# Kernel tuning notes

Hardware: AMD Instinct MI355X
Metric: run time of the kernel (lower is better)

The kernel has to match this reference:

```python
import jax, jax.numpy as jnp
import numpy as np

WH, WW = 8, 8          # window height/width
N = WH * WW            # tokens per window = 64
DIM = 256              # channels
H = 8                  # heads
HD = DIM // H          # head dim = 32
NW = 1024              # number of windows per image (256/8)^2
B_ = 4096              # num_windows * batch (batch=4)
EPS = 1e-12            # F.normalize eps


def _rel_pos_index():
    # (2,Wh,Ww) coords -> pairwise relative index into bias table, shape (N, N)
    coords = np.stack(np.meshgrid(np.arange(WH), np.arange(WW), indexing='ij'))
    flat = coords.reshape(2, -1)                      # (2, N)
    rel = flat[:, :, None] - flat[:, None, :]         # (2, N, N)
    rel = rel.transpose(1, 2, 0).astype(np.int64)     # (N, N, 2)
    rel[..., 0] += WH - 1
    rel[..., 1] += WW - 1
    rel[..., 0] *= 2 * WW - 1
    return jnp.asarray(rel.sum(-1))                   # (N, N)

_RPI = _rel_pos_index()


def setup_inputs() -> dict:
    key = jax.random.key(0)
    ks = jax.random.split(key, 12)
    x = jax.random.normal(ks[0], (B_, N, DIM), dtype=jnp.float32)
    c = jax.random.normal(ks[1], (B_, N, DIM), dtype=jnp.float32)
    # 0 / -100 additive shifted-window mask, shape (nW, N, N)
    mask = jnp.where(jax.random.uniform(ks[2], (NW, N, N)) < 0.15, -100.0, 0.0).astype(jnp.float32)
    q_w = jax.random.normal(ks[3], (DIM, DIM), dtype=jnp.float32) * 0.02
    q_b = jnp.zeros((DIM,), jnp.float32)
    kv_w = jax.random.normal(ks[4], (2 * DIM, DIM), dtype=jnp.float32) * 0.02
    kv_b = jnp.zeros((2 * DIM,), jnp.float32)
    logit_scale = jnp.log(10.0) * jnp.ones((H, 1, 1), jnp.float32)
    rpb_table = jax.random.normal(ks[5], ((2 * WH - 1) * (2 * WW - 1), H), dtype=jnp.float32) * 0.02
    proj_w = jax.random.normal(ks[6], (DIM, DIM), dtype=jnp.float32) * 0.02
    proj_b = jnp.zeros((DIM,), jnp.float32)
    return {"x": x, "c": c, "mask": mask, "q_w": q_w, "q_b": q_b,
            "kv_w": kv_w, "kv_b": kv_b, "logit_scale": logit_scale,
            "rpb_table": rpb_table, "proj_w": proj_w, "proj_b": proj_b}


def _l2norm(t):
    n = jnp.sqrt(jnp.sum(t * t, axis=-1, keepdims=True))
    return t / jnp.maximum(n, EPS)


def reference(x, c, mask, q_w, q_b, kv_w, kv_b, logit_scale, rpb_table, proj_w, proj_b):
    Bw, n, Cdim = x.shape
    q = (x @ q_w.T + q_b).reshape(Bw, n, H, HD).transpose(0, 2, 1, 3)      # (B_,H,N,hd)
    kv = (c @ kv_w.T + kv_b).reshape(Bw, n, 2, H, HD).transpose(2, 0, 3, 1, 4)
    k, v = kv[0], kv[1]                                                     # (B_,H,N,hd)
    # cosine-similarity attention with learned clamped logit scale
    attn = jnp.einsum('bhnd,bhmd->bhnm', _l2norm(q), _l2norm(k))
    scale = jnp.exp(jnp.minimum(logit_scale, jnp.log(1.0 / 0.01)))          # (H,1,1)
    attn = attn * scale[None]
    # relative position bias gather: (N,N,H) -> (H,N,N)
    bias = rpb_table[_RPI.reshape(-1)].reshape(n, n, H).transpose(2, 0, 1)
    attn = attn + bias[None]
    # shifted-window mask
    attn = attn.reshape(Bw // NW, NW, H, n, n) + mask[None, :, None]
    attn = jax.nn.softmax(attn.reshape(Bw, H, n, n), axis=-1)
    out = jnp.einsum('bhnm,bhmd->bhnd', attn, v).transpose(0, 2, 1, 3).reshape(Bw, n, Cdim)
    return out @ proj_w.T + proj_b
```

## Files before the change

kernel.cpp:

```cpp
#include <hip/hip_runtime.h>
#include <hip/hip_bf16.h>


typedef __attribute__((ext_vector_type(4))) float f32x4;
typedef __attribute__((ext_vector_type(8))) short bf16x8;
typedef __attribute__((ext_vector_type(4))) unsigned int u32x4;

#define MFMA16(a, b, c) __builtin_amdgcn_mfma_f32_16x16x32_bf16((a), (b), (c), 0, 0, 0)

union FragAB {
  bf16x8 v;
  ushort u[8];
  u32x4  q4;
};

__device__ __forceinline__ ushort f2b(float f) {
  union { float f; unsigned int u; } cv; cv.f = f;
  unsigned int u = cv.u;
  return (ushort)((u + 0x7fffu + ((u >> 16) & 1u)) >> 16);
}

__device__ __forceinline__ bf16x8 ldfrag(const ushort* p) {
  FragAB f;
  f.q4 = *(const u32x4*)p;
  return f.v;
}

__device__ __forceinline__ f32x4 fzero() {
  f32x4 z = {0.0f, 0.0f, 0.0f, 0.0f};
  return z;
}

__global__ void prep_kernel(const float* __restrict__ qw, const float* __restrict__ kvw,
                            const float* __restrict__ pw, const float* __restrict__ rpb,
                            const float* __restrict__ lsc,
                            ushort* __restrict__ qwb, ushort* __restrict__ kvwb,
                            ushort* __restrict__ pwb, float* __restrict__ biasT,
                            float* __restrict__ scale) {
  int t = blockIdx.x * blockDim.x + threadIdx.x;
  int stride = gridDim.x * blockDim.x;
  for (int i = t; i < 256 * 256; i += stride) {
    int o = i >> 8, rem = i & 255;
    int kg = rem >> 5, r2 = rem & 31, lg = r2 >> 3, e = r2 & 7;
    int k = (kg << 5) + (lg << 2) + (e < 4 ? e : e + 12);
    qwb[i] = f2b(qw[(o << 8) + k]);
    pwb[i] = f2b(pw[(o << 8) + k]);
  }
  for (int i = t; i < 512 * 256; i += stride) {
    int o = i >> 8, rem = i & 255;
    int kg = rem >> 5, r2 = rem & 31, lg = r2 >> 3, e = r2 & 7;
    int k = (kg << 5) + (lg << 2) + (e < 4 ? e : e + 12);
    kvwb[i] = f2b(kvw[(o << 8) + k]);
  }
  for (int i = t; i < 8 * 64 * 64; i += stride) {
    int h = i >> 12, m = (i >> 6) & 63, n = i & 63;
    int idx = ((n >> 3) - (m >> 3) + 7) * 15 + ((n & 7) - (m & 7) + 7);
    biasT[i] = rpb[idx * 8 + h];
  }
  if (t < 8) scale[t] = __expf(fminf(lsc[t], 4.6051701859880914f));
}

__global__ __launch_bounds__(512, 2)
void wattn_fused(const float* __restrict__ xg, const float* __restrict__ cg,
                 const float* __restrict__ maskg,
                 const float* __restrict__ qb, const float* __restrict__ kvb,
                 const float* __restrict__ pb,
                 const ushort* __restrict__ qwb, const ushort* __restrict__ kvwb,
                 const ushort* __restrict__ pwb,
                 const float* __restrict__ biasT, const float* __restrict__ scaleg,
                 float* __restrict__ outg) {
  __shared__ ushort xs[64][264];
  __shared__ ushort qs[64][264];
  __shared__ ushort ks[64][264];
  __shared__ ushort vts[256][72];
  __shared__ float  ms[64][65];

  const int b    = blockIdx.x;
  const int wid  = b & 1023;
  const int tid  = threadIdx.x;
  const int w    = tid >> 6;
  const int lane = tid & 63;
  const int lg   = lane >> 4;
  const int lc   = lane & 15;
  const int c0   = w << 5;

  {
    const float4* src = (const float4*)(xg + (size_t)b * 16384);
#pragma unroll
    for (int it = 0; it < 8; ++it) {
      int i = tid + it * 512;
      float4 v = src[i];
      int row = i >> 6;
      int col = (i & 63) << 2;
      ushort* p = &xs[row][(col & ~31) + (((col & 15) >> 2) << 3) + ((col & 16) ? 4 : 0)];
      p[0] = f2b(v.x); p[1] = f2b(v.y); p[2] = f2b(v.z); p[3] = f2b(v.w);
    }
    const float* mp = maskg + (size_t)wid * 4096;
#pragma unroll
    for (int it = 0; it < 8; ++it) {
      int i = tid + it * 512;
      ms[i & 63][i >> 6] = mp[i];
    }
  }
  __syncthreads();

  {
    f32x4 acc[4][2];
#pragma unroll
    for (int mt = 0; mt < 4; ++mt)
#pragma unroll
      for (int nt = 0; nt < 2; ++nt) acc[mt][nt] = fzero();
#pragma unroll
    for (int kg = 0; kg < 8; ++kg) {
      bf16x8 a[4], bb[2];
#pragma unroll
      for (int mt = 0; mt < 4; ++mt)
        a[mt] = ldfrag(&xs[mt * 16 + lc][(kg << 5) + (lg << 3)]);
#pragma unroll
      for (int nt = 0; nt < 2; ++nt)
        bb[nt] = ldfrag(qwb + ((c0 + nt * 16 + lc) << 8) + (kg << 5) + (lg << 3));
#pragma unroll
      for (int mt = 0; mt < 4; ++mt)
#pragma unroll
        for (int nt = 0; nt < 2; ++nt)
          acc[mt][nt] = MFMA16(a[mt], bb[nt], acc[mt][nt]);
    }
    float bias0 = qb[c0 + lc], bias1 = qb[c0 + 16 + lc];
    const int cp0 = c0 + ((lc >> 2) << 3) + (lc & 3);
#pragma unroll
    for (int mt = 0; mt < 4; ++mt) {
#pragma unroll
      for (int reg = 0; reg < 4; ++reg) {
        float v0 = acc[mt][0][reg] + bias0;
        float v1 = acc[mt][1][reg] + bias1;
        float ss = v0 * v0 + v1 * v1;
        ss += __shfl_xor(ss, 1);
        ss += __shfl_xor(ss, 2);
        ss += __shfl_xor(ss, 4);
        ss += __shfl_xor(ss, 8);
        float inv = 1.0f / fmaxf(sqrtf(ss), 1e-12f);
        int row = mt * 16 + (lg << 2) + reg;
        qs[row][cp0]     = f2b(v0 * inv);
        qs[row][cp0 + 4] = f2b(v1 * inv);
      }
    }
  }
  __syncthreads();

  {
    const float4* src = (const float4*)(cg + (size_t)b * 16384);
#pragma unroll
    for (int it = 0; it < 8; ++it) {
      int i = tid + it * 512;
      float4 v = src[i];
      int row = i >> 6;
      int col = (i & 63) << 2;
      ushort* p = &xs[row][(col & ~31) + (((col & 15) >> 2) << 3) + ((col & 16) ? 4 : 0)];
      p[0] = f2b(v.x); p[1] = f2b(v.y); p[2] = f2b(v.z); p[3] = f2b(v.w);
    }
  }
  __syncthreads();

  {
#pragma unroll
    for (int pass = 0; pass < 2; ++pass) {
      const int o0 = (pass << 8) + c0;
      f32x4 acc[4][2];
#pragma unroll
      for (int mt = 0; mt < 4; ++mt)
#pragma unroll
        for (int nt = 0; nt < 2; ++nt) acc[mt][nt] = fzero();
#pragma unroll
      for (int kg = 0; kg < 8; ++kg) {
        bf16x8 a[4], bb[2];
#pragma unroll
        for (int mt = 0; mt < 4; ++mt)
          a[mt] = ldfrag(&xs[mt * 16 + lc][(kg << 5) + (lg << 3)]);
#pragma unroll
        for (int nt = 0; nt < 2; ++nt)
          bb[nt] = ldfrag(kvwb + ((o0 + nt * 16 + lc) << 8) + (kg << 5) + (lg << 3));
#pragma unroll
        for (int mt = 0; mt < 4; ++mt)
#pragma unroll
          for (int nt = 0; nt < 2; ++nt)
            acc[mt][nt] = MFMA16(a[mt], bb[nt], acc[mt][nt]);
      }
      float bias0 = kvb[o0 + lc], bias1 = kvb[o0 + 16 + lc];
      if (pass == 0) {
        const int cp0 = c0 + ((lc >> 2) << 3) + (lc & 3);
#pragma unroll
        for (int mt = 0; mt < 4; ++mt) {
#pragma unroll
          for (int reg = 0; reg < 4; ++reg) {
            float v0 = acc[mt][0][reg] + bias0;
            float v1 = acc[mt][1][reg] + bias1;
            float ss = v0 * v0 + v1 * v1;
            ss += __shfl_xor(ss, 1);
            ss += __shfl_xor(ss, 2);
            ss += __shfl_xor(ss, 4);
            ss += __shfl_xor(ss, 8);
            float inv = 1.0f / fmaxf(sqrtf(ss), 1e-12f);
            int row = mt * 16 + (lg << 2) + reg;
            ks[row][cp0]     = f2b(v0 * inv);
            ks[row][cp0 + 4] = f2b(v1 * inv);
          }
        }
      } else {
#pragma unroll
        for (int mt = 0; mt < 4; ++mt) {
#pragma unroll
          for (int reg = 0; reg < 4; ++reg) {
            int mpk = ((mt >> 1) << 5) + (lg << 3) + reg + ((mt & 1) ? 4 : 0);
            vts[c0 + lc][mpk]      = f2b(acc[mt][0][reg] + bias0);
            vts[c0 + 16 + lc][mpk] = f2b(acc[mt][1][reg] + bias1);
          }
        }
      }
    }
  }
  __syncthreads();

  {
    const int h = w;
    const float sc = scaleg[h];
    f32x4 st[4][4];
#pragma unroll
    for (int mt = 0; mt < 4; ++mt)
#pragma unroll
      for (int nt = 0; nt < 4; ++nt) st[mt][nt] = fzero();
    {
      bf16x8 a[4], bq[4];
#pragma unroll
      for (int t4 = 0; t4 < 4; ++t4) {
        a[t4]  = ldfrag(&ks[t4 * 16 + lc][(h << 5) + (lg << 3)]);
        bq[t4] = ldfrag(&qs[t4 * 16 + lc][(h << 5) + (lg << 3)]);
      }
#pragma unroll
      for (int mt = 0; mt < 4; ++mt)
#pragma unroll
        for (int nt = 0; nt < 4; ++nt)
          st[mt][nt] = MFMA16(a[mt], bq[nt], st[mt][nt]);
    }
    const float* bT = biasT + (h << 12);
#pragma unroll
    for (int nt = 0; nt < 4; ++nt) {
      int n = nt * 16 + lc;
      float mx = -3.0e38f;
#pragma unroll
      for (int mt = 0; mt < 4; ++mt)
#pragma unroll
        for (int reg = 0; reg < 4; ++reg) {
          int m = mt * 16 + (lg << 2) + reg;
          float val = st[mt][nt][reg] * sc + bT[(m << 6) + n] + ms[m][n];
          st[mt][nt][reg] = val;
          mx = fmaxf(mx, val);
        }
      mx = fmaxf(mx, __shfl_xor(mx, 16));
      mx = fmaxf(mx, __shfl_xor(mx, 32));
      float sm = 0.0f;
#pragma unroll
      for (int mt = 0; mt < 4; ++mt)
#pragma unroll
        for (int reg = 0; reg < 4; ++reg) {
          float e = __expf(st[mt][nt][reg] - mx);
          st[mt][nt][reg] = e;
          sm += e;
        }
      sm += __shfl_xor(sm, 16);
      sm += __shfl_xor(sm, 32);
      float inv = 1.0f / sm;
#pragma unroll
      for (int mt = 0; mt < 4; ++mt)
#pragma unroll
        for (int reg = 0; reg < 4; ++reg) st[mt][nt][reg] *= inv;
    }
    f32x4 ot[2][4];
#pragma unroll
    for (int dmt = 0; dmt < 2; ++dmt)
#pragma unroll
      for (int nt = 0; nt < 4; ++nt) ot[dmt][nt] = fzero();
#pragma unroll
    for (int kt = 0; kt < 2; ++kt) {
      bf16x8 av[2];
#pragma unroll
      for (int dmt = 0; dmt < 2; ++dmt)
        av[dmt] = ldfrag(&vts[(h << 5) + dmt * 16 + lc][(kt << 5) + (lg << 3)]);
#pragma unroll
      for (int nt = 0; nt < 4; ++nt) {
        FragAB bp;
#pragma unroll
        for (int j = 0; j < 4; ++j) {
          bp.u[j]     = f2b(st[2 * kt][nt][j]);
          bp.u[4 + j] = f2b(st[2 * kt + 1][nt][j]);
        }
#pragma unroll
        for (int dmt = 0; dmt < 2; ++dmt)
          ot[dmt][nt] = MFMA16(av[dmt], bp.v, ot[dmt][nt]);
      }
    }
#pragma unroll
    for (int dmt = 0; dmt < 2; ++dmt)
#pragma unroll
      for (int nt = 0; nt < 4; ++nt)
#pragma unroll
        for (int reg = 0; reg < 4; ++reg) {
          int n = nt * 16 + lc;
          xs[n][(h << 5) + (lg << 3) + reg + (dmt ? 4 : 0)] = f2b(ot[dmt][nt][reg]);
        }
  }
  __syncthreads();

  {
    f32x4 acc[4][2];
#pragma unroll
    for (int mt = 0; mt < 4; ++mt)
#pragma unroll
      for (int nt = 0; nt < 2; ++nt) acc[mt][nt] = fzero();
#pragma unroll
    for (int kg = 0; kg < 8; ++kg) {
      bf16x8 a[4], bb[2];
#pragma unroll
      for (int mt = 0; mt < 4; ++mt)
        a[mt] = ldfrag(&xs[mt * 16 + lc][(kg << 5) + (lg << 3)]);
#pragma unroll
      for (int nt = 0; nt < 2; ++nt)
        bb[nt] = ldfrag(pwb + ((c0 + nt * 16 + lc) << 8) + (kg << 5) + (lg << 3));
#pragma unroll
      for (int mt = 0; mt < 4; ++mt)
#pragma unroll
        for (int nt = 0; nt < 2; ++nt)
          acc[mt][nt] = MFMA16(a[mt], bb[nt], acc[mt][nt]);
    }
    float bias0 = pb[c0 + lc], bias1 = pb[c0 + 16 + lc];
    float* op = outg + (size_t)b * 16384;
#pragma unroll
    for (int mt = 0; mt < 4; ++mt) {
#pragma unroll
      for (int reg = 0; reg < 4; ++reg) {
        int row = mt * 16 + (lg << 2) + reg;
        op[(row << 8) + c0 + lc]      = acc[mt][0][reg] + bias0;
        op[(row << 8) + c0 + 16 + lc] = acc[mt][1][reg] + bias1;
      }
    }
  }
}

extern "C" void kernel_launch(void* const* d_in, const int* in_sizes, int n_in,
                              void* d_out, int out_size, void* d_ws, size_t ws_size,
                              hipStream_t stream) {
  const float* x    = (const float*)d_in[0];
  const float* c    = (const float*)d_in[1];
  const float* mask = (const float*)d_in[2];
  const float* q_w  = (const float*)d_in[3];
  const float* q_b  = (const float*)d_in[4];
  const float* kv_w = (const float*)d_in[5];
  const float* kv_b = (const float*)d_in[6];
  const float* lsc  = (const float*)d_in[7];
  const float* rpb  = (const float*)d_in[8];
  const float* p_w  = (const float*)d_in[9];
  const float* p_b  = (const float*)d_in[10];

  char* ws = (char*)d_ws;
  ushort* qwb   = (ushort*)(ws);
  ushort* kvwb  = (ushort*)(ws + 131072);
  ushort* pwb   = (ushort*)(ws + 131072 + 262144);
  float*  biasT = (float*)(ws + 524288);
  float*  scale = (float*)(ws + 524288 + 131072);

  prep_kernel<<<64, 256, 0, stream>>>(q_w, kv_w, p_w, rpb, lsc, qwb, kvwb, pwb, biasT, scale);
  wattn_fused<<<4096, 512, 0, stream>>>(x, c, mask, q_b, kv_b, p_b, qwb, kvwb, pwb,
                                        biasT, scale, (float*)d_out);
}
```

Before: 522.1 us.

## Keep per-head Q/K/V in registers and per-wave scratch to cut LDS and raise occupancy

Each wave now computes only its own head's Q, K and V columns and keeps normalized Q/K fragments in registers, staging through a small per-wave LDS scratch instead of shared full-size q/k/vT buffers. The mask is stored as bf16 and the launch bound is raised to four blocks per CU, which cuts LDS use enough to allow more resident blocks. Cross-wave barriers between the KV projection and attention are removed, but register pressure rises under the tighter launch bound, which may cause spills. The float-to-bf16 conversion now uses the HIP intrinsic, and the V store is packed into 64-bit writes.

```diff
diff --git a/kernel.cpp b/kernel.cpp
--- a/kernel.cpp
+++ b/kernel.cpp
@@ -5,6 +5,8 @@
 typedef __attribute__((ext_vector_type(4))) float f32x4;
 typedef __attribute__((ext_vector_type(8))) short bf16x8;
 typedef __attribute__((ext_vector_type(4))) unsigned int u32x4;
+typedef __attribute__((ext_vector_type(2))) unsigned int u32x2;
+typedef __attribute__((ext_vector_type(4))) unsigned short u16x4;
 
 #define MFMA16(a, b, c) __builtin_amdgcn_mfma_f32_16x16x32_bf16((a), (b), (c), 0, 0, 0)
 
@@ -12,17 +14,31 @@
   bf16x8 v;
   ushort u[8];
   u32x4  q4;
+  u32x2  q2[2];
 };
 
 __device__ __forceinline__ ushort f2b(float f) {
-  union { float f; unsigned int u; } cv; cv.f = f;
-  unsigned int u = cv.u;
-  return (ushort)((u + 0x7fffu + ((u >> 16) & 1u)) >> 16);
+  union { __hip_bfloat16 h; ushort u; } cv;
+  cv.h = __float2bfloat16(f);
+  return cv.u;
+}
+
+__device__ __forceinline__ float b2f(ushort u) {
+  union { float f; unsigned int x; } cv;
+  cv.x = ((unsigned)u) << 16;
+  return cv.f;
 }
 
 __device__ __forceinline__ bf16x8 ldfrag(const ushort* p) {
   FragAB f;
   f.q4 = *(const u32x4*)p;
+  return f.v;
+}
+
+__device__ __forceinline__ bf16x8 ldfrag8(const ushort* p) {
+  FragAB f;
+  f.q2[0] = *(const u32x2*)p;
+  f.q2[1] = *(const u32x2*)(p + 4);
   return f.v;
 }
 
@@ -60,7 +76,7 @@
   if (t < 8) scale[t] = __expf(fminf(lsc[t], 4.6051701859880914f));
 }
 
-__global__ __launch_bounds__(512, 2)
+__global__ __launch_bounds__(512, 4)
 void wattn_fused(const float* __restrict__ xg, const float* __restrict__ cg,
                  const float* __restrict__ maskg,
                  const float* __restrict__ qb, const float* __restrict__ kvb,
@@ -69,11 +85,9 @@
                  const ushort* __restrict__ pwb,
                  const float* __restrict__ biasT, const float* __restrict__ scaleg,
                  float* __restrict__ outg) {
-  __shared__ ushort xs[64][264];
-  __shared__ ushort qs[64][264];
-  __shared__ ushort ks[64][264];
-  __shared__ ushort vts[256][72];
-  __shared__ float  ms[64][65];
+  __shared__ __align__(16) ushort xs[64][264];
+  __shared__ __align__(16) ushort scr[8][64][36];
+  __shared__ __align__(16) ushort msb[64][66];
 
   const int b    = blockIdx.x;
   const int wid  = b & 1023;
@@ -84,6 +98,9 @@
   const int lc   = lane & 15;
   const int c0   = w << 5;
 
+  ushort (*myscr)[36] = scr[w];
+  ushort (*vscr)[72]  = (ushort(*)[72])&scr[w][0][0];
+
   {
     const float4* src = (const float4*)(xg + (size_t)b * 16384);
 #pragma unroll
@@ -99,11 +116,14 @@
 #pragma unroll
     for (int it = 0; it < 8; ++it) {
       int i = tid + it * 512;
-      ms[i & 63][i >> 6] = mp[i];
+      msb[i & 63][i >> 6] = f2b(mp[i]);
     }
   }
   __syncthreads();
 
+  const int cp0 = ((lc >> 2) << 3) + (lc & 3);
+
+  bf16x8 qf[4];
   {
     f32x4 acc[4][2];
 #pragma unroll
@@ -126,7 +146,6 @@
           acc[mt][nt] = MFMA16(a[mt], bb[nt], acc[mt][nt]);
     }
     float bias0 = qb[c0 + lc], bias1 = qb[c0 + 16 + lc];
-    const int cp0 = c0 + ((lc >> 2) << 3) + (lc & 3);
 #pragma unroll
     for (int mt = 0; mt < 4; ++mt) {
 #pragma unroll
@@ -140,10 +159,13 @@
         ss += __shfl_xor(ss, 8);
         float inv = 1.0f / fmaxf(sqrtf(ss), 1e-12f);
         int row = mt * 16 + (lg << 2) + reg;
-        qs[row][cp0]     = f2b(v0 * inv);
-        qs[row][cp0 + 4] = f2b(v1 * inv);
-      }
-    }
+        myscr[row][cp0]     = f2b(v0 * inv);
+        myscr[row][cp0 + 4] = f2b(v1 * inv);
+      }
+    }
+#pragma unroll
+    for (int t4 = 0; t4 < 4; ++t4)
+      qf[t4] = ldfrag8(&myscr[t4 * 16 + lc][lg << 3]);
   }
   __syncthreads();
 
@@ -161,87 +183,102 @@
   }
   __syncthreads();
 
-  {
-#pragma unroll
-    for (int pass = 0; pass < 2; ++pass) {
-      const int o0 = (pass << 8) + c0;
-      f32x4 acc[4][2];
-#pragma unroll
-      for (int mt = 0; mt < 4; ++mt)
-#pragma unroll
-        for (int nt = 0; nt < 2; ++nt) acc[mt][nt] = fzero();
-#pragma unroll
-      for (int kg = 0; kg < 8; ++kg) {
-        bf16x8 a[4], bb[2];
-#pragma unroll
-        for (int mt = 0; mt < 4; ++mt)
-          a[mt] = ldfrag(&xs[mt * 16 + lc][(kg << 5) + (lg << 3)]);
+  bf16x8 kf[4];
+  {
+    f32x4 acc[4][2];
+#pragma unroll
+    for (int mt = 0; mt < 4; ++mt)
+#pragma unroll
+      for (int nt = 0; nt < 2; ++nt) acc[mt][nt] = fzero();
+#pragma unroll
+    for (int kg = 0; kg < 8; ++kg) {
+      bf16x8 a[4], bb[2];
+#pragma unroll
+      for (int mt = 0; mt < 4; ++mt)
+        a[mt] = ldfrag(&xs[mt * 16 + lc][(kg << 5) + (lg << 3)]);
+#pragma unroll
+      for (int nt = 0; nt < 2; ++nt)
+        bb[nt] = ldfrag(kvwb + ((c0 + nt * 16 + lc) << 8) + (kg << 5) + (lg << 3));
+#pragma unroll
+      for (int mt = 0; mt < 4; ++mt)
 #pragma unroll
         for (int nt = 0; nt < 2; ++nt)
-          bb[nt] = ldfrag(kvwb + ((o0 + nt * 16 + lc) << 8) + (kg << 5) + (lg << 3));
-#pragma unroll
-        for (int mt = 0; mt < 4; ++mt)
-#pragma unroll
-          for (int nt = 0; nt < 2; ++nt)
-            acc[mt][nt] = MFMA16(a[mt], bb[nt], acc[mt][nt]);
-      }
-      float bias0 = kvb[o0 + lc], bias1 = kvb[o0 + 16 + lc];
-      if (pass == 0) {
-        const int cp0 = c0 + ((lc >> 2) << 3) + (lc & 3);
-#pragma unroll
-        for (int mt = 0; mt < 4; ++mt) {
-#pragma unroll
-          for (int reg = 0; reg < 4; ++reg) {
-            float v0 = acc[mt][0][reg] + bias0;
-            float v1 = acc[mt][1][reg] + bias1;
-            float ss = v0 * v0 + v1 * v1;
-            ss += __shfl_xor(ss, 1);
-            ss += __shfl_xor(ss, 2);
-            ss += __shfl_xor(ss, 4);
-            ss += __shfl_xor(ss, 8);
-            float inv = 1.0f / fmaxf(sqrtf(ss), 1e-12f);
-            int row = mt * 16 + (lg << 2) + reg;
-            ks[row][cp0]     = f2b(v0 * inv);
-            ks[row][cp0 + 4] = f2b(v1 * inv);
-          }
-        }
-      } else {
-#pragma unroll
-        for (int mt = 0; mt < 4; ++mt) {
-#pragma unroll
-          for (int reg = 0; reg < 4; ++reg) {
-            int mpk = ((mt >> 1) << 5) + (lg << 3) + reg + ((mt & 1) ? 4 : 0);
-            vts[c0 + lc][mpk]      = f2b(acc[mt][0][reg] + bias0);
-            vts[c0 + 16 + lc][mpk] = f2b(acc[mt][1][reg] + bias1);
-          }
-        }
-      }
-    }
-  }
-  __syncthreads();
-
-  {
-    const int h = w;
-    const float sc = scaleg[h];
+          acc[mt][nt] = MFMA16(a[mt], bb[nt], acc[mt][nt]);
+    }
+    float bias0 = kvb[c0 + lc], bias1 = kvb[c0 + 16 + lc];
+#pragma unroll
+    for (int mt = 0; mt < 4; ++mt) {
+#pragma unroll
+      for (int reg = 0; reg < 4; ++reg) {
+        float v0 = acc[mt][0][reg] + bias0;
+        float v1 = acc[mt][1][reg] + bias1;
+        float ss = v0 * v0 + v1 * v1;
+        ss += __shfl_xor(ss, 1);
+        ss += __shfl_xor(ss, 2);
+        ss += __shfl_xor(ss, 4);
+        ss += __shfl_xor(ss, 8);
+        float inv = 1.0f / fmaxf(sqrtf(ss), 1e-12f);
+        int row = mt * 16 + (lg << 2) + reg;
+        myscr[row][cp0]     = f2b(v0 * inv);
+        myscr[row][cp0 + 4] = f2b(v1 * inv);
+      }
+    }
+#pragma unroll
+    for (int t4 = 0; t4 < 4; ++t4)
+      kf[t4] = ldfrag8(&myscr[t4 * 16 + lc][lg << 3]);
+  }
+
+  {
+    f32x4 acc[4][2];
+#pragma unroll
+    for (int mt = 0; mt < 4; ++mt)
+#pragma unroll
+      for (int nt = 0; nt < 2; ++nt) acc[mt][nt] = fzero();
+#pragma unroll
+    for (int kg = 0; kg < 8; ++kg) {
+      bf16x8 a[4], bb[2];
+#pragma unroll
+      for (int mt = 0; mt < 4; ++mt)
+        a[mt] = ldfrag(&xs[mt * 16 + lc][(kg << 5) + (lg << 3)]);
+#pragma unroll
+      for (int nt = 0; nt < 2; ++nt)
+        bb[nt] = ldfrag(kvwb + ((256 + c0 + nt * 16 + lc) << 8) + (kg << 5) + (lg << 3));
+#pragma unroll
+      for (int mt = 0; mt < 4; ++mt)
+#pragma unroll
+        for (int nt = 0; nt < 2; ++nt)
+          acc[mt][nt] = MFMA16(a[mt], bb[nt], acc[mt][nt]);
+    }
+    float bias0 = kvb[256 + c0 + lc], bias1 = kvb[256 + c0 + 16 + lc];
+#pragma unroll
+    for (int mt = 0; mt < 4; ++mt) {
+      int off = ((mt >> 1) << 5) | (lg << 3) | ((mt & 1) << 2);
+      u16x4 pk0, pk1;
+#pragma unroll
+      for (int reg = 0; reg < 4; ++reg) {
+        pk0[reg] = f2b(acc[mt][0][reg] + bias0);
+        pk1[reg] = f2b(acc[mt][1][reg] + bias1);
+      }
+      *(u16x4*)&vscr[lc][off]      = pk0;
+      *(u16x4*)&vscr[16 + lc][off] = pk1;
+    }
+  }
+
+  f32x4 ot[2][4];
+  {
+    const float sc = scaleg[w];
     f32x4 st[4][4];
 #pragma unroll
     for (int mt = 0; mt < 4; ++mt)
 #pragma unroll
       for (int nt = 0; nt < 4; ++nt) st[mt][nt] = fzero();
-    {
-      bf16x8 a[4], bq[4];
-#pragma unroll
-      for (int t4 = 0; t4 < 4; ++t4) {
-        a[t4]  = ldfrag(&ks[t4 * 16 + lc][(h << 5) + (lg << 3)]);
-        bq[t4] = ldfrag(&qs[t4 * 16 + lc][(h << 5) + (lg << 3)]);
-      }
-#pragma unroll
-      for (int mt = 0; mt < 4; ++mt)
-#pragma unroll
-        for (int nt = 0; nt < 4; ++nt)
-          st[mt][nt] = MFMA16(a[mt], bq[nt], st[mt][nt]);
-    }
-    const float* bT = biasT + (h << 12);
+#pragma unroll
+    for (int mt = 0; mt < 4; ++mt)
+#pragma unroll
+      for (int nt = 0; nt < 4; ++nt)
+        st[mt][nt] = MFMA16(kf[mt], qf[nt], st[mt][nt]);
+
+    const float* bT = biasT + (w << 12);
 #pragma unroll
     for (int nt = 0; nt < 4; ++nt) {
       int n = nt * 16 + lc;
@@ -251,7 +288,7 @@
 #pragma unroll
         for (int reg = 0; reg < 4; ++reg) {
           int m = mt * 16 + (lg << 2) + reg;
-          float val = st[mt][nt][reg] * sc + bT[(m << 6) + n] + ms[m][n];
+          float val = st[mt][nt][reg] * sc + bT[(m << 6) + n] + b2f(msb[m][n]);
           st[mt][nt][reg] = val;
           mx = fmaxf(mx, val);
         }
@@ -274,7 +311,7 @@
 #pragma unroll
         for (int reg = 0; reg < 4; ++reg) st[mt][nt][reg] *= inv;
     }
-    f32x4 ot[2][4];
+
 #pragma unroll
     for (int dmt = 0; dmt < 2; ++dmt)
 #pragma unroll
@@ -284,7 +321,7 @@
       bf16x8 av[2];
 #pragma unroll
       for (int dmt = 0; dmt < 2; ++dmt)
-        av[dmt] = ldfrag(&vts[(h << 5) + dmt * 16 + lc][(kt << 5) + (lg << 3)]);
+        av[dmt] = ldfrag(&vscr[dmt * 16 + lc][(kt << 5) + (lg << 3)]);
 #pragma unroll
       for (int nt = 0; nt < 4; ++nt) {
         FragAB bp;
@@ -298,16 +335,18 @@
           ot[dmt][nt] = MFMA16(av[dmt], bp.v, ot[dmt][nt]);
       }
     }
-#pragma unroll
-    for (int dmt = 0; dmt < 2; ++dmt)
-#pragma unroll
-      for (int nt = 0; nt < 4; ++nt)
-#pragma unroll
-        for (int reg = 0; reg < 4; ++reg) {
-          int n = nt * 16 + lc;
-          xs[n][(h << 5) + (lg << 3) + reg + (dmt ? 4 : 0)] = f2b(ot[dmt][nt][reg]);
-        }
-  }
+  }
+  __syncthreads();
+
+#pragma unroll
+  for (int dmt = 0; dmt < 2; ++dmt)
+#pragma unroll
+    for (int nt = 0; nt < 4; ++nt)
+#pragma unroll
+      for (int reg = 0; reg < 4; ++reg) {
+        int n = nt * 16 + lc;
+        xs[n][c0 + (lg << 3) + reg + (dmt ? 4 : 0)] = f2b(ot[dmt][nt][reg]);
+      }
   __syncthreads();
 
   {
```

Result: slower. 541.7 us (+3.8%).
